# Performance work log

Measured on AMD Instinct MI355X. Metric: run time of the kernel, lower is better.

Reference implementation:

```python
import jax, jax.numpy as jnp
import numpy as np

B, N, D = 16, 2048, 64


def setup_inputs() -> dict:
    key = jax.random.key(0)
    kq, kk, kv = jax.random.split(key, 3)
    queries = jax.random.normal(kq, (B, N, D), dtype=jnp.float32)
    keys = jax.random.normal(kk, (B, N, D), dtype=jnp.float32)
    values = jax.random.normal(kv, (B, N, D), dtype=jnp.float32)
    return {"queries": queries, "keys": keys, "values": values}


def reference(queries, keys, values):
    d = queries.shape[-1]
    scale = 1.0 / jnp.sqrt(jnp.asarray(d, dtype=queries.dtype))
    # scores: [B, N, N] = Q @ K^T / sqrt(d)
    scores = jnp.einsum("bqd,bkd->bqk", queries, keys) * scale
    attn = jax.nn.softmax(scores, axis=-1)
    # dropout prob = 0.0 -> identity (inference-faithful)
    out = jnp.einsum("bqk,bkd->bqd", attn, values)
    return out
```

## Files before the change

### kernel.cpp

```cpp
#include <hip/hip_runtime.h>

typedef __attribute__((ext_vector_type(8)))  __bf16 bf16x8;
typedef __attribute__((ext_vector_type(4)))  __bf16 bf16x4;
typedef __attribute__((ext_vector_type(16))) float  f32x16;
typedef __attribute__((ext_vector_type(4)))  float  f32x4;

#define B_    16
#define N_    2048
#define D_    64
#define QBLK  128
#define KVBLK 32
#define NT    (N_ / KVBLK)
#define NG    4
#define TPG   (NT / NG)
#define NP    (TPG / 2)

#define VSTR    72
#define KSZ     4096
#define SLOT_SZ 8704
#define GRP_SZ  (4 * SLOT_SZ)
#define SMEM_SZ (NG * GRP_SZ)

static __device__ __forceinline__ float fast_exp2(float x) {
#if __has_builtin(__builtin_amdgcn_exp2f)
    return __builtin_amdgcn_exp2f(x);
#else
    return __expf(x * 0.6931471805599453f);
#endif
}

__global__ __attribute__((amdgpu_waves_per_eu(4, 4))) __launch_bounds__(1024)
void attn_fwd(const float* __restrict__ Qp, const float* __restrict__ Kp,
              const float* __restrict__ Vp, float* __restrict__ Op)
{
    __shared__ __align__(16) char smem[SMEM_SZ];

    const int tid  = threadIdx.x;
    const int g    = tid >> 8;
    const int tg   = tid & 255;
    const int lane = tid & 63;
    const int w    = (tid >> 6) & 3;
    const int h    = lane >> 5;
    const int qcol = lane & 31;

    const int bx    = blockIdx.x;
    const int batch = ((bx & 7) << 1) | ((bx >> 3) & 1);
    const int qtile = bx >> 4;
    const int q0w   = qtile * QBLK + w * 32;

    const float SL2E = 0.18033688011112042f;
    const size_t bboff = (size_t)batch * (N_ * D_);
    char* gbase = smem + g * GRP_SZ;

    const float* qrow = Qp + bboff + (size_t)(q0w + qcol) * D_ + h * 8;
    bf16x8 qf[4];
#pragma unroll
    for (int m = 0; m < 4; ++m) {
        f32x4 a = *reinterpret_cast<const f32x4*>(qrow + m * 16);
        f32x4 b = *reinterpret_cast<const f32x4*>(qrow + m * 16 + 4);
#pragma unroll
        for (int j = 0; j < 4; ++j) { qf[m][j] = (__bf16)a[j]; qf[m][4 + j] = (__bf16)b[j]; }
    }

    const int krow = tg >> 3,  kcol = (tg & 7) * 8;
    const int vrow = tg & 31,  vcol = (tg >> 5) * 8;
    const float* ksrc0 = Kp + bboff + (size_t)krow * D_ + kcol;
    const float* vsrc0 = Vp + bboff + (size_t)vrow * D_ + vcol;

    f32x4 kr[2], vr[2];
    auto load_tile = [&](int t) {
        const float* ks = ksrc0 + (size_t)t * KVBLK * D_;
        const float* vs = vsrc0 + (size_t)t * KVBLK * D_;
        kr[0] = *reinterpret_cast<const f32x4*>(ks);
        kr[1] = *reinterpret_cast<const f32x4*>(ks + 4);
        vr[0] = *reinterpret_cast<const f32x4*>(vs);
        vr[1] = *reinterpret_cast<const f32x4*>(vs + 4);
    };

    auto write_tile = [&](int b) {
        char* kb = gbase + b * SLOT_SZ;
        char* vb = kb + KSZ;
        bf16x8 w0;
#pragma unroll
        for (int j = 0; j < 4; ++j) { w0[j] = (__bf16)kr[0][j]; w0[4 + j] = (__bf16)kr[1][j]; }
        *reinterpret_cast<bf16x8*>(kb + krow * 128 + ((kcol * 2) ^ ((krow & 7) << 4))) = w0;
#pragma unroll 8
        for (int i = 0; i < 8; ++i) {
            const int d = vcol + i;
            *reinterpret_cast<__bf16*>(vb + d * VSTR + vrow * 2) =
                (__bf16)vr[i >> 2][i & 3];
        }
    };

    f32x16 o0, o1;
#pragma unroll
    for (int i = 0; i < 16; ++i) { o0[i] = 0.f; o1[i] = 0.f; }
    float l_run = 0.f;

    const int kx = (qcol & 7) << 4;

    auto qk_tile = [&](const char* kb, f32x16& s) {
#pragma unroll
        for (int m = 0; m < 4; ++m) {
            const int col = m * 32 + h * 16;
            bf16x8 k0 = *reinterpret_cast<const bf16x8*>(kb + qcol * 128 + (col ^ kx));
            s = __builtin_amdgcn_mfma_f32_32x32x16_bf16(k0, qf[m], s, 0, 0, 0);
        }
    };
    auto exp_tile = [&](const f32x16& s, bf16x8& pfa, bf16x8& pfb) {
        float ps0 = 0.f, ps1 = 0.f, ps2 = 0.f, ps3 = 0.f;
#pragma unroll
        for (int i = 0; i < 4; ++i) {
            float p0 = fast_exp2(s[i]      * SL2E);
            float p1 = fast_exp2(s[4 + i]  * SL2E);
            float p2 = fast_exp2(s[8 + i]  * SL2E);
            float p3 = fast_exp2(s[12 + i] * SL2E);
            ps0 += p0; ps1 += p1; ps2 += p2; ps3 += p3;
            pfa[i] = (__bf16)p0; pfa[4 + i] = (__bf16)p1;
            pfb[i] = (__bf16)p2; pfb[4 + i] = (__bf16)p3;
        }
        l_run += (ps0 + ps1) + (ps2 + ps3);
    };
    auto pv_tile = [&](const char* vb, const bf16x8& pfa, const bf16x8& pfb) {
#pragma unroll
        for (int db = 0; db < 2; ++db) {
            const int drow = db * 32 + qcol;
            const char* vrowp = vb + drow * VSTR;
            f32x16& oo = db ? o1 : o0;
#pragma unroll
            for (int sub = 0; sub < 2; ++sub) {
                const int cb = sub * 32 + h * 8;
                bf16x4 v0 = *reinterpret_cast<const bf16x4*>(vrowp + cb);
                bf16x4 v1 = *reinterpret_cast<const bf16x4*>(vrowp + cb + 16);
                bf16x8 vf;
#pragma unroll
                for (int j = 0; j < 4; ++j) { vf[j] = v0[j]; vf[4 + j] = v1[j]; }
                oo = __builtin_amdgcn_mfma_f32_32x32x16_bf16(vf, sub ? pfb : pfa, oo, 0, 0, 0);
            }
        }
    };

    load_tile(g);          write_tile(0);
    load_tile(NG + g);     write_tile(1);
    __syncthreads();

    for (int p = 0; p < NP; ++p) {
        const int cur  = (p & 1) * 2;
        const int nxt  = cur ^ 2;
        const bool more = (p + 1 < NP);
        if (more) load_tile(NG * (2 * p + 2) + g);

        const char* kbA = gbase + cur * SLOT_SZ;        const char* vbA = kbA + KSZ;
        const char* kbB = gbase + (cur + 1) * SLOT_SZ;  const char* vbB = kbB + KSZ;

        f32x16 sA, sB;
#pragma unroll
        for (int i = 0; i < 16; ++i) { sA[i] = 0.f; sB[i] = 0.f; }
        __builtin_amdgcn_s_setprio(1);
        qk_tile(kbA, sA);
        qk_tile(kbB, sB);
        __builtin_amdgcn_s_setprio(0);

        bf16x8 paA, pbA;
        exp_tile(sA, paA, pbA);
        __builtin_amdgcn_s_setprio(1);
        pv_tile(vbA, paA, pbA);
        __builtin_amdgcn_s_setprio(0);

        if (more) { write_tile(nxt); load_tile(NG * (2 * p + 3) + g); }

        bf16x8 paB, pbB;
        exp_tile(sB, paB, pbB);
        __builtin_amdgcn_s_setprio(1);
        pv_tile(vbB, paB, pbB);
        __builtin_amdgcn_s_setprio(0);

        if (more) write_tile(nxt + 1);
        __syncthreads();
    }

    float lt = l_run + __shfl_xor(l_run, 32);
    float* mlF  = (float*)smem;
    float* slab = (float*)smem;
    const int q  = w * 32 + qcol;

    if (h == 0) mlF[g * QBLK + q] = lt;
    __syncthreads();

    const float L = mlF[0 * QBLK + q] + mlF[1 * QBLK + q]
                  + mlF[2 * QBLK + q] + mlF[3 * QBLK + q];
    const float inv = 1.0f / L;
    __syncthreads();

    const int dl0 = 4 * h;
    auto slab_write = [&](float* sb, const f32x16& oo, int db) {
#pragma unroll
        for (int r = 0; r < 16; ++r) {
            const int d = db * 32 + (r & 3) + 8 * (r >> 2) + dl0;
            sb[d * 128 + q] = oo[r];
        }
    };
    auto slab_add = [&](const float* sb, f32x16& oo, int db) {
#pragma unroll
        for (int r = 0; r < 16; ++r) {
            const int d = db * 32 + (r & 3) + 8 * (r >> 2) + dl0;
            oo[r] += sb[d * 128 + q];
        }
    };

    if (g == 1) { slab_write(slab, o0, 0);        slab_write(slab, o1, 1); }
    if (g == 3) { slab_write(slab + 8192, o0, 0); slab_write(slab + 8192, o1, 1); }
    __syncthreads();

    if (g == 0) { slab_add(slab, o0, 0);        slab_add(slab, o1, 1); }
    if (g == 2) { slab_add(slab + 8192, o0, 0); slab_add(slab + 8192, o1, 1); }
    __syncthreads();

    if (g == 2) { slab_write(slab, o0, 0); slab_write(slab, o1, 1); }
    __syncthreads();

    if (g == 0) {
#pragma unroll
        for (int r = 0; r < 16; ++r) {
            const int d0 = (r & 3) + 8 * (r >> 2) + dl0;
            o0[r] = (o0[r] + slab[d0 * 128 + q]) * inv;
            o1[r] = (o1[r] + slab[(32 + d0) * 128 + q]) * inv;
        }
        float* orow = Op + bboff + (size_t)(q0w + qcol) * D_;
#pragma unroll
        for (int gg8 = 0; gg8 < 4; ++gg8) {
            f32x4 v, v2;
#pragma unroll
            for (int r = 0; r < 4; ++r) { v[r] = o0[4 * gg8 + r]; v2[r] = o1[4 * gg8 + r]; }
            *reinterpret_cast<f32x4*>(orow + gg8 * 8 + 4 * h)      = v;
            *reinterpret_cast<f32x4*>(orow + 32 + gg8 * 8 + 4 * h) = v2;
        }
    }
}

extern "C" void kernel_launch(void* const* d_in, const int* in_sizes, int n_in,
                              void* d_out, int out_size, void* d_ws, size_t ws_size,
                              hipStream_t stream) {
    const float* Q = (const float*)d_in[0];
    const float* K = (const float*)d_in[1];
    const float* V = (const float*)d_in[2];
    float* O = (float*)d_out;
    dim3 grid(256), block(1024);
    hipLaunchKernelGGL(attn_fwd, grid, block, 0, stream, Q, K, V, O);
}
```

Before: 41.13 us.

## Permute V smem layout for single 16-byte reads and fold scale into Q

The V tile in shared memory is now stored with a permuted key-column order and a wider row stride, so each PV MFMA operand comes from one bf16x8 load instead of two bf16x4 loads plus a shuffle. The softmax scale times log2(e) is applied to Q once at load, which removes a multiply per score element in the exp stage. The loop goes from processing two KV tiles per barrier with a four-slot buffer to one tile per barrier with double buffering. That halves shared memory use but doubles the number of __syncthreads and shortens the interleaved QK/exp/PV pipeline. Scaling Q before the bf16 conversion slightly changes rounding.

```diff
diff --git a/kernel.cpp b/kernel.cpp
--- a/kernel.cpp
+++ b/kernel.cpp
@@ -1,7 +1,6 @@
 #include <hip/hip_runtime.h>
 
 typedef __attribute__((ext_vector_type(8)))  __bf16 bf16x8;
-typedef __attribute__((ext_vector_type(4)))  __bf16 bf16x4;
 typedef __attribute__((ext_vector_type(16))) float  f32x16;
 typedef __attribute__((ext_vector_type(4)))  float  f32x4;
 
@@ -13,12 +12,11 @@
 #define NT    (N_ / KVBLK)
 #define NG    4
 #define TPG   (NT / NG)
-#define NP    (TPG / 2)
-
-#define VSTR    72
+
+#define VSTR    80
 #define KSZ     4096
-#define SLOT_SZ 8704
-#define GRP_SZ  (4 * SLOT_SZ)
+#define SLOT_SZ (KSZ + 64 * VSTR)
+#define GRP_SZ  (2 * SLOT_SZ)
 #define SMEM_SZ (NG * GRP_SZ)
 
 static __device__ __forceinline__ float fast_exp2(float x) {
@@ -59,11 +57,16 @@
         f32x4 a = *reinterpret_cast<const f32x4*>(qrow + m * 16);
         f32x4 b = *reinterpret_cast<const f32x4*>(qrow + m * 16 + 4);
 #pragma unroll
-        for (int j = 0; j < 4; ++j) { qf[m][j] = (__bf16)a[j]; qf[m][4 + j] = (__bf16)b[j]; }
+        for (int j = 0; j < 4; ++j) {
+            qf[m][j]     = (__bf16)(a[j] * SL2E);
+            qf[m][4 + j] = (__bf16)(b[j] * SL2E);
+        }
     }
 
     const int krow = tg >> 3,  kcol = (tg & 7) * 8;
     const int vrow = tg & 31,  vcol = (tg >> 5) * 8;
+    const int vin  = vrow & 15;
+    const int vpos = ((vrow >> 4) * 2 + ((vin >> 2) & 1)) * 8 + (vin & 3) + 4 * (vin >> 3);
     const float* ksrc0 = Kp + bboff + (size_t)krow * D_ + kcol;
     const float* vsrc0 = Vp + bboff + (size_t)vrow * D_ + vcol;
 
@@ -87,7 +90,7 @@
 #pragma unroll 8
         for (int i = 0; i < 8; ++i) {
             const int d = vcol + i;
-            *reinterpret_cast<__bf16*>(vb + d * VSTR + vrow * 2) =
+            *reinterpret_cast<__bf16*>(vb + d * VSTR + vpos * 2) =
                 (__bf16)vr[i >> 2][i & 3];
         }
     };
@@ -99,83 +102,58 @@
 
     const int kx = (qcol & 7) << 4;
 
-    auto qk_tile = [&](const char* kb, f32x16& s) {
+    load_tile(g);
+    write_tile(0);
+    __syncthreads();
+
+    for (int it = 0; it < TPG; ++it) {
+        const int cur = it & 1;
+        if (it + 1 < TPG) load_tile(NG * (it + 1) + g);
+
+        const char* kb = gbase + cur * SLOT_SZ;
+        const char* vb = kb + KSZ;
+
+        f32x16 s;
+#pragma unroll
+        for (int i = 0; i < 16; ++i) s[i] = 0.f;
+        __builtin_amdgcn_s_setprio(1);
 #pragma unroll
         for (int m = 0; m < 4; ++m) {
             const int col = m * 32 + h * 16;
             bf16x8 k0 = *reinterpret_cast<const bf16x8*>(kb + qcol * 128 + (col ^ kx));
             s = __builtin_amdgcn_mfma_f32_32x32x16_bf16(k0, qf[m], s, 0, 0, 0);
         }
-    };
-    auto exp_tile = [&](const f32x16& s, bf16x8& pfa, bf16x8& pfb) {
+        __builtin_amdgcn_s_setprio(0);
+
         float ps0 = 0.f, ps1 = 0.f, ps2 = 0.f, ps3 = 0.f;
+        bf16x8 pfa, pfb;
 #pragma unroll
         for (int i = 0; i < 4; ++i) {
-            float p0 = fast_exp2(s[i]      * SL2E);
-            float p1 = fast_exp2(s[4 + i]  * SL2E);
-            float p2 = fast_exp2(s[8 + i]  * SL2E);
-            float p3 = fast_exp2(s[12 + i] * SL2E);
+            float p0 = fast_exp2(s[i]);
+            float p1 = fast_exp2(s[4 + i]);
+            float p2 = fast_exp2(s[8 + i]);
+            float p3 = fast_exp2(s[12 + i]);
             ps0 += p0; ps1 += p1; ps2 += p2; ps3 += p3;
             pfa[i] = (__bf16)p0; pfa[4 + i] = (__bf16)p1;
             pfb[i] = (__bf16)p2; pfb[4 + i] = (__bf16)p3;
         }
         l_run += (ps0 + ps1) + (ps2 + ps3);
-    };
-    auto pv_tile = [&](const char* vb, const bf16x8& pfa, const bf16x8& pfb) {
+
+        if (it + 1 < TPG) write_tile(cur ^ 1);
+
+        __builtin_amdgcn_s_setprio(1);
 #pragma unroll
         for (int db = 0; db < 2; ++db) {
-            const int drow = db * 32 + qcol;
-            const char* vrowp = vb + drow * VSTR;
+            const char* vrowp = vb + (db * 32 + qcol) * VSTR + h * 16;
             f32x16& oo = db ? o1 : o0;
 #pragma unroll
             for (int sub = 0; sub < 2; ++sub) {
-                const int cb = sub * 32 + h * 8;
-                bf16x4 v0 = *reinterpret_cast<const bf16x4*>(vrowp + cb);
-                bf16x4 v1 = *reinterpret_cast<const bf16x4*>(vrowp + cb + 16);
-                bf16x8 vf;
-#pragma unroll
-                for (int j = 0; j < 4; ++j) { vf[j] = v0[j]; vf[4 + j] = v1[j]; }
+                bf16x8 vf = *reinterpret_cast<const bf16x8*>(vrowp + sub * 32);
                 oo = __builtin_amdgcn_mfma_f32_32x32x16_bf16(vf, sub ? pfb : pfa, oo, 0, 0, 0);
             }
         }
-    };
-
-    load_tile(g);          write_tile(0);
-    load_tile(NG + g);     write_tile(1);
-    __syncthreads();
-
-    for (int p = 0; p < NP; ++p) {
-        const int cur  = (p & 1) * 2;
-        const int nxt  = cur ^ 2;
-        const bool more = (p + 1 < NP);
-        if (more) load_tile(NG * (2 * p + 2) + g);
-
-        const char* kbA = gbase + cur * SLOT_SZ;        const char* vbA = kbA + KSZ;
-        const char* kbB = gbase + (cur + 1) * SLOT_SZ;  const char* vbB = kbB + KSZ;
-
-        f32x16 sA, sB;
-#pragma unroll
-        for (int i = 0; i < 16; ++i) { sA[i] = 0.f; sB[i] = 0.f; }
-        __builtin_amdgcn_s_setprio(1);
-        qk_tile(kbA, sA);
-        qk_tile(kbB, sB);
         __builtin_amdgcn_s_setprio(0);
 
-        bf16x8 paA, pbA;
-        exp_tile(sA, paA, pbA);
-        __builtin_amdgcn_s_setprio(1);
-        pv_tile(vbA, paA, pbA);
-        __builtin_amdgcn_s_setprio(0);
-
-        if (more) { write_tile(nxt); load_tile(NG * (2 * p + 3) + g); }
-
-        bf16x8 paB, pbB;
-        exp_tile(sB, paB, pbB);
-        __builtin_amdgcn_s_setprio(1);
-        pv_tile(vbB, paB, pbB);
-        __builtin_amdgcn_s_setprio(0);
-
-        if (more) write_tile(nxt + 1);
         __syncthreads();
     }
 
```

Result: faster. 37.11 us (-9.8%).
